# Kernel tuning notes

Hardware: AMD Instinct MI355X
Metric: run time of the kernel (lower is better)

Reference implementation:

```python
import jax, jax.numpy as jnp
import numpy as np

B, P, N, D = 8, 4, 1024, 384
H, PD = 8, 48  # num_heads, projection_dim = D // H
SCALE = float(PD ** 0.5)


def setup_inputs() -> dict:
    key = jax.random.key(0)
    ks = jax.random.split(key, 3)
    x = jax.random.normal(ks[0], (B, P, N, D), dtype=jnp.float32)
    w_qkv = jax.random.normal(ks[1], (D, H, 3 * PD), dtype=jnp.float32) * (1.0 / np.sqrt(D))
    b_qkv = jnp.zeros((H, 3 * PD), dtype=jnp.float32)
    w_o = jax.random.normal(ks[2], (PD, H, D), dtype=jnp.float32) * (1.0 / np.sqrt(PD * H))
    b_o = jnp.zeros((D,), dtype=jnp.float32)
    return {"x": x, "w_qkv": w_qkv, "b_qkv": b_qkv, "w_o": w_o, "b_o": b_o}


def reference(x, w_qkv, b_qkv, w_o, b_o):
    # QKV projection: [b,p,n,d] x [d,h,3e] -> [b,p,h,n,3e]
    qkv = jnp.einsum('bpnd,dhe->bphne', x, w_qkv) + b_qkv[None, None, :, None, :]
    q, k, v = jnp.split(qkv, 3, axis=-1)  # each [b,p,h,n,e]
    # attention over n (patches) within each (b,p,h)
    attn = jnp.einsum('bphie,bphje->bphij', q, k) / SCALE
    attn = jax.nn.softmax(attn, axis=-1)
    wv = jnp.einsum('bphij,bphje->bphie', attn, v)  # [b,p,h,n,e]
    out = jnp.einsum('bphne,ehd->bpnd', wv, w_o) + b_o
    return out
```

## Files before the change

### kernel.cpp

```cpp
#include <hip/hip_runtime.h>
#include <hip/hip_bf16.h>


#define BP 32
#define NN 1024
#define DD 384
#define HH 8
#define PDIM 48
#define E3 144
#define OO 1152
#define EP 64
#define MTOT (BP * NN)

typedef unsigned short u16;
typedef __attribute__((ext_vector_type(8))) short short8;
typedef __attribute__((ext_vector_type(4))) float f32x4;

__device__ __forceinline__ u16 f2bf(float f) {
    union { float f; unsigned int u; } v;
    v.f = f;
    unsigned int u = v.u;
    unsigned int r = u + 0x7FFFu + ((u >> 16) & 1u);
    return (u16)(r >> 16);
}

__device__ __forceinline__ void gload16(const u16* g, u16* l) {
    __builtin_amdgcn_global_load_lds(
        (const __attribute__((address_space(1))) void*)g,
        (__attribute__((address_space(3))) void*)l, 16, 0, 0);
}

__global__ void prep_kernel(const float* __restrict__ x,
                            const float* __restrict__ w_qkv,
                            const float* __restrict__ w_o,
                            u16* __restrict__ Wt, u16* __restrict__ Wot,
                            u16* __restrict__ xb) {
    int stride = gridDim.x * blockDim.x;
    int t0 = blockIdx.x * blockDim.x + threadIdx.x;
    for (int i = t0; i < OO * DD; i += stride) {
        int o = i / DD, d = i - o * DD;
        Wt[i] = f2bf(w_qkv[(size_t)d * OO + o]);
    }
    for (int i = t0; i < DD * DD; i += stride) {
        int dd = i / DD, he = i - dd * DD;
        int h = he / PDIM, e = he - h * PDIM;
        Wot[i] = f2bf(w_o[((size_t)e * HH + h) * DD + dd]);
    }
    for (int i = t0; i < MTOT * DD / 8; i += stride) {
        const float4* xp = reinterpret_cast<const float4*>(x + (size_t)i * 8);
        float4 a0 = xp[0], a1 = xp[1];
        short8 v;
        v[0] = (short)f2bf(a0.x); v[1] = (short)f2bf(a0.y);
        v[2] = (short)f2bf(a0.z); v[3] = (short)f2bf(a0.w);
        v[4] = (short)f2bf(a1.x); v[5] = (short)f2bf(a1.y);
        v[6] = (short)f2bf(a1.z); v[7] = (short)f2bf(a1.w);
        reinterpret_cast<short8*>(xb)[i] = v;
    }
}

__device__ __forceinline__ void stage_tile(const u16* __restrict__ src, int ld,
                                           u16* lds, int tid) {
#pragma unroll
    for (int i = 0; i < 4; ++i) {
        int idx = i * 256 + tid;
        int row = idx >> 3, p = idx & 7;
        int g = p ^ (row & 7);
        gload16(src + (size_t)row * ld + g * 8, lds + idx * 8);
    }
}
__device__ __forceinline__ short8 lds_frag(const u16* lds, int row, int kk, int lg) {
    int p = (kk * 4 + lg) ^ (row & 7);
    return *reinterpret_cast<const short8*>(lds + row * 64 + p * 8);
}

__global__ __launch_bounds__(256) void qkv_kernel(
    const u16* __restrict__ xb, const float* __restrict__ b_qkv,
    const u16* __restrict__ Wt,
    u16* __restrict__ q_ws, u16* __restrict__ k_ws, u16* __restrict__ vt_ws) {
    __shared__ alignas(16) u16 Al[128 * 64];
    __shared__ alignas(16) u16 Bl[128 * 64];
    int mt = blockIdx.x, nt = blockIdx.y;
    int tid = threadIdx.x;
    int w = tid >> 6, l = tid & 63, lr = l & 15, lg = l >> 4;
    int wr = w >> 1, wc = w & 1;

    const u16* Abase = xb + (size_t)mt * 128 * DD;
    const u16* Bbase = Wt + (size_t)nt * 128 * DD;

    f32x4 acc[4][4];
#pragma unroll
    for (int mi = 0; mi < 4; ++mi)
#pragma unroll
        for (int ni = 0; ni < 4; ++ni) acc[mi][ni] = (f32x4)(0.f);

#pragma unroll 1
    for (int kt = 0; kt < 6; ++kt) {
        __syncthreads();
        stage_tile(Abase + kt * 64, DD, Al, tid);
        stage_tile(Bbase + kt * 64, DD, Bl, tid);
        __syncthreads();
#pragma unroll
        for (int kk = 0; kk < 2; ++kk) {
            short8 a[4], b[4];
#pragma unroll
            for (int mi = 0; mi < 4; ++mi) a[mi] = lds_frag(Al, wr * 64 + mi * 16 + lr, kk, lg);
#pragma unroll
            for (int ni = 0; ni < 4; ++ni) b[ni] = lds_frag(Bl, wc * 64 + ni * 16 + lr, kk, lg);
#pragma unroll
            for (int mi = 0; mi < 4; ++mi)
#pragma unroll
                for (int ni = 0; ni < 4; ++ni)
                    acc[mi][ni] = __builtin_amdgcn_mfma_f32_16x16x32_bf16(a[mi], b[ni], acc[mi][ni], 0, 0, 0);
        }
    }

#pragma unroll
    for (int ni = 0; ni < 4; ++ni) {
        int o = nt * 128 + wc * 64 + ni * 16 + lr;
        int h = o / E3, e3 = o - h * E3;
        float bias = b_qkv[o];
#pragma unroll
        for (int mi = 0; mi < 4; ++mi)
#pragma unroll
            for (int r = 0; r < 4; ++r) {
                int M = mt * 128 + wr * 64 + mi * 16 + lg * 4 + r;
                int bp = M >> 10, nn = M & 1023;
                size_t bh = (size_t)bp * HH + h;
                u16 bv = f2bf(acc[mi][ni][r] + bias);
                if (e3 < 48) {
                    size_t base = (bh * NN + nn) * EP;
                    q_ws[base + e3] = bv;
                    if (e3 < 16) q_ws[base + 48 + e3] = 0;
                } else if (e3 < 96) {
                    int c = e3 - 48;
                    size_t base = (bh * NN + nn) * EP;
                    k_ws[base + c] = bv;
                    if (c < 16) k_ws[base + 48 + c] = 0;
                } else {
                    vt_ws[(bh * PDIM + (e3 - 96)) * NN + nn] = bv;
                }
            }
    }
}

__global__ __launch_bounds__(256) void attn_kernel(
    const u16* __restrict__ q_ws, const u16* __restrict__ k_ws,
    const u16* __restrict__ vt_ws, u16* __restrict__ wv_ws) {
    int rt = blockIdx.x;
    int bph = blockIdx.y;
    int bp = bph >> 3, h = bph & 7;
    int tid = threadIdx.x;
    int w = tid >> 6, l = tid & 63;
    int lr = l & 15, lg = l >> 4;

    __shared__ alignas(16) u16 Klds[64][72];
    __shared__ alignas(16) u16 Vlds[48][72];
    __shared__ alignas(16) u16 Plds[4][16][72];

    int qn = rt * 64 + w * 16 + lr;
    const u16* qrow = q_ws + ((size_t)bph * NN + qn) * EP;
    short8 aq0 = *reinterpret_cast<const short8*>(qrow + lg * 8);
    short8 aq1 = *reinterpret_cast<const short8*>(qrow + 32 + lg * 8);

    f32x4 accO[3];
#pragma unroll
    for (int i = 0; i < 3; ++i) accO[i] = (f32x4)(0.f);
    float mrun[4], lrun[4];
#pragma unroll
    for (int r = 0; r < 4; ++r) { mrun[r] = -1e30f; lrun[r] = 0.f; }
    const float inv_scale = 0.14433756729740643f;

#pragma unroll 1
    for (int jc = 0; jc < 16; ++jc) {
        {
            int j = tid >> 2, seg = (tid & 3) * 16;
            const u16* src = k_ws + ((size_t)bph * NN + jc * 64 + j) * EP + seg;
            *reinterpret_cast<short8*>(&Klds[j][seg]) = *reinterpret_cast<const short8*>(src);
            *reinterpret_cast<short8*>(&Klds[j][seg + 8]) = *reinterpret_cast<const short8*>(src + 8);
            if (tid < 192) {
                int e = tid >> 2;
                const u16* vsrc = vt_ws + ((size_t)bph * PDIM + e) * NN + jc * 64 + seg;
                *reinterpret_cast<short8*>(&Vlds[e][seg]) = *reinterpret_cast<const short8*>(vsrc);
                *reinterpret_cast<short8*>(&Vlds[e][seg + 8]) = *reinterpret_cast<const short8*>(vsrc + 8);
            }
        }
        __syncthreads();

        f32x4 s[4];
#pragma unroll
        for (int ct = 0; ct < 4; ++ct) {
            s[ct] = (f32x4)(0.f);
            short8 bk0 = *reinterpret_cast<const short8*>(&Klds[ct * 16 + lr][lg * 8]);
            short8 bk1 = *reinterpret_cast<const short8*>(&Klds[ct * 16 + lr][32 + lg * 8]);
            s[ct] = __builtin_amdgcn_mfma_f32_16x16x32_bf16(aq0, bk0, s[ct], 0, 0, 0);
            s[ct] = __builtin_amdgcn_mfma_f32_16x16x32_bf16(aq1, bk1, s[ct], 0, 0, 0);
        }
#pragma unroll
        for (int ct = 0; ct < 4; ++ct) s[ct] *= inv_scale;

        float mnew[4], alpha[4];
#pragma unroll
        for (int r = 0; r < 4; ++r) {
            float m = fmaxf(fmaxf(s[0][r], s[1][r]), fmaxf(s[2][r], s[3][r]));
#pragma unroll
            for (int off = 1; off < 16; off <<= 1) m = fmaxf(m, __shfl_xor(m, off));
            mnew[r] = fmaxf(mrun[r], m);
            alpha[r] = __expf(mrun[r] - mnew[r]);
            mrun[r] = mnew[r];
        }
        float p[4][4];
#pragma unroll
        for (int ct = 0; ct < 4; ++ct)
#pragma unroll
            for (int r = 0; r < 4; ++r) p[ct][r] = __expf(s[ct][r] - mnew[r]);
#pragma unroll
        for (int r = 0; r < 4; ++r) {
            float rs = p[0][r] + p[1][r] + p[2][r] + p[3][r];
#pragma unroll
            for (int off = 1; off < 16; off <<= 1) rs += __shfl_xor(rs, off);
            lrun[r] = lrun[r] * alpha[r] + rs;
        }
#pragma unroll
        for (int i = 0; i < 3; ++i)
#pragma unroll
            for (int r = 0; r < 4; ++r) accO[i][r] *= alpha[r];

#pragma unroll
        for (int ct = 0; ct < 4; ++ct)
#pragma unroll
            for (int r = 0; r < 4; ++r)
                Plds[w][lg * 4 + r][ct * 16 + lr] = f2bf(p[ct][r]);

#pragma unroll
        for (int kb = 0; kb < 2; ++kb) {
            short8 ap = *reinterpret_cast<const short8*>(&Plds[w][lr][kb * 32 + lg * 8]);
#pragma unroll
            for (int et = 0; et < 3; ++et) {
                short8 bv = *reinterpret_cast<const short8*>(&Vlds[et * 16 + lr][kb * 32 + lg * 8]);
                accO[et] = __builtin_amdgcn_mfma_f32_16x16x32_bf16(ap, bv, accO[et], 0, 0, 0);
            }
        }
        __syncthreads();
    }

#pragma unroll
    for (int et = 0; et < 3; ++et)
#pragma unroll
        for (int r = 0; r < 4; ++r) {
            int nn = rt * 64 + w * 16 + lg * 4 + r;
            int he = h * PDIM + et * 16 + lr;
            wv_ws[((size_t)bp * NN + nn) * DD + he] = f2bf(accO[et][r] / lrun[r]);
        }
}

__global__ __launch_bounds__(256) void oproj_kernel(
    const u16* __restrict__ wv_ws, const u16* __restrict__ Wot,
    const float* __restrict__ b_o, float* __restrict__ out) {
    __shared__ alignas(16) u16 Al[128 * 64];
    __shared__ alignas(16) u16 Bl[128 * 64];
    int mt = blockIdx.x, nt = blockIdx.y;
    int tid = threadIdx.x;
    int w = tid >> 6, l = tid & 63, lr = l & 15, lg = l >> 4;
    int wr = w >> 1, wc = w & 1;

    const u16* Abase = wv_ws + (size_t)mt * 128 * DD;
    const u16* Bbase = Wot + (size_t)nt * 128 * DD;

    f32x4 acc[4][4];
#pragma unroll
    for (int mi = 0; mi < 4; ++mi)
#pragma unroll
        for (int ni = 0; ni < 4; ++ni) acc[mi][ni] = (f32x4)(0.f);

#pragma unroll 1
    for (int kt = 0; kt < 6; ++kt) {
        __syncthreads();
        stage_tile(Abase + kt * 64, DD, Al, tid);
        stage_tile(Bbase + kt * 64, DD, Bl, tid);
        __syncthreads();
#pragma unroll
        for (int kk = 0; kk < 2; ++kk) {
            short8 a[4], b[4];
#pragma unroll
            for (int mi = 0; mi < 4; ++mi) a[mi] = lds_frag(Al, wr * 64 + mi * 16 + lr, kk, lg);
#pragma unroll
            for (int ni = 0; ni < 4; ++ni) b[ni] = lds_frag(Bl, wc * 64 + ni * 16 + lr, kk, lg);
#pragma unroll
            for (int mi = 0; mi < 4; ++mi)
#pragma unroll
                for (int ni = 0; ni < 4; ++ni)
                    acc[mi][ni] = __builtin_amdgcn_mfma_f32_16x16x32_bf16(a[mi], b[ni], acc[mi][ni], 0, 0, 0);
        }
    }

#pragma unroll
    for (int ni = 0; ni < 4; ++ni) {
        int d = nt * 128 + wc * 64 + ni * 16 + lr;
        float bo = b_o[d];
#pragma unroll
        for (int mi = 0; mi < 4; ++mi)
#pragma unroll
            for (int r = 0; r < 4; ++r) {
                int M = mt * 128 + wr * 64 + mi * 16 + lg * 4 + r;
                out[(size_t)M * DD + d] = acc[mi][ni][r] + bo;
            }
    }
}

extern "C" void kernel_launch(void* const* d_in, const int* in_sizes, int n_in,
                              void* d_out, int out_size, void* d_ws, size_t ws_size,
                              hipStream_t stream) {
    const float* x     = (const float*)d_in[0];
    const float* w_qkv = (const float*)d_in[1];
    const float* b_qkv = (const float*)d_in[2];
    const float* w_o   = (const float*)d_in[3];
    const float* b_o   = (const float*)d_in[4];
    float* out = (float*)d_out;

    char* ws = (char*)d_ws;
    size_t off = 0;
    u16* Wt    = (u16*)(ws + off); off += (size_t)OO * DD * 2;
    u16* Wot   = (u16*)(ws + off); off += (size_t)DD * DD * 2;
    u16* q_ws  = (u16*)(ws + off); off += (size_t)BP * HH * NN * EP * 2;
    u16* k_ws  = (u16*)(ws + off); off += (size_t)BP * HH * NN * EP * 2;
    u16* vt_ws = (u16*)(ws + off); off += (size_t)BP * HH * PDIM * NN * 2;
    u16* wv_ws = (u16*)(ws + off); off += (size_t)BP * NN * DD * 2;
    u16* xb    = wv_ws;
    (void)ws_size;

    prep_kernel<<<2048, 256, 0, stream>>>(x, w_qkv, w_o, Wt, Wot, xb);
    qkv_kernel<<<dim3(256, 9), 256, 0, stream>>>(xb, b_qkv, Wt, q_ws, k_ws, vt_ws);
    attn_kernel<<<dim3(16, 256), 256, 0, stream>>>(q_ws, k_ws, vt_ws, wv_ws);
    oproj_kernel<<<dim3(256, 3), 256, 0, stream>>>(wv_ws, Wot, b_o, out);
}
```

Baseline: 408.1 us.

## Restructure attention: 128-row tiles, async swizzled LDS loads, lazy softmax rescale

Each attention workgroup now handles 128 query rows instead of 64, with each wave holding two 16-row Q fragments. Every K/V fragment read from LDS therefore feeds two MFMAs, and the number of K/V tile loads per query is halved. K and V tiles are staged with direct global-to-LDS loads into an XOR-swizzled layout, which removes the padding; V rows are padded to 64 so the loads come out uniform. The softmax scale is folded into Q inside the QKV epilogue, and the running-max rescale is skipped when the new max exceeds the old one by no more than 8. The grid is also remapped to a 1D block order spread across XCDs, at the cost of a larger V workspace and more registers per thread.

```diff
diff --git a/kernel.cpp b/kernel.cpp
--- a/kernel.cpp
+++ b/kernel.cpp
@@ -10,6 +10,7 @@
 #define E3 144
 #define OO 1152
 #define EP 64
+#define VROWS 64
 #define MTOT (BP * NN)
 
 typedef unsigned short u16;
@@ -22,6 +23,12 @@
     unsigned int u = v.u;
     unsigned int r = u + 0x7FFFu + ((u >> 16) & 1u);
     return (u16)(r >> 16);
+}
+
+__device__ __forceinline__ u16 f2bf_hw(float f) {
+    union { __hip_bfloat16 b; u16 u; } v;
+    v.b = __float2bfloat16(f);
+    return v.u;
 }
 
 __device__ __forceinline__ void gload16(const u16* g, u16* l) {
@@ -114,6 +121,7 @@
         }
     }
 
+    const float inv_scale = 0.14433756729740643f;
 #pragma unroll
     for (int ni = 0; ni < 4; ++ni) {
         int o = nt * 128 + wc * 64 + ni * 16 + lr;
@@ -126,18 +134,18 @@
                 int M = mt * 128 + wr * 64 + mi * 16 + lg * 4 + r;
                 int bp = M >> 10, nn = M & 1023;
                 size_t bh = (size_t)bp * HH + h;
-                u16 bv = f2bf(acc[mi][ni][r] + bias);
+                float val = acc[mi][ni][r] + bias;
                 if (e3 < 48) {
                     size_t base = (bh * NN + nn) * EP;
-                    q_ws[base + e3] = bv;
+                    q_ws[base + e3] = f2bf(val * inv_scale);
                     if (e3 < 16) q_ws[base + 48 + e3] = 0;
                 } else if (e3 < 96) {
                     int c = e3 - 48;
                     size_t base = (bh * NN + nn) * EP;
-                    k_ws[base + c] = bv;
+                    k_ws[base + c] = f2bf(val);
                     if (c < 16) k_ws[base + 48 + c] = 0;
                 } else {
-                    vt_ws[(bh * PDIM + (e3 - 96)) * NN + nn] = bv;
+                    vt_ws[(bh * VROWS + (e3 - 96)) * NN + nn] = f2bf(val);
                 }
             }
     }
@@ -146,111 +154,133 @@
 __global__ __launch_bounds__(256) void attn_kernel(
     const u16* __restrict__ q_ws, const u16* __restrict__ k_ws,
     const u16* __restrict__ vt_ws, u16* __restrict__ wv_ws) {
-    int rt = blockIdx.x;
-    int bph = blockIdx.y;
-    int bp = bph >> 3, h = bph & 7;
+    int bid = blockIdx.x;
+    int wgid = (bid & 7) * 256 + (bid >> 3);
+    int bph = wgid >> 3, rt = wgid & 7;
+    int bp = bph >> 3, hd = bph & 7;
     int tid = threadIdx.x;
-    int w = tid >> 6, l = tid & 63;
-    int lr = l & 15, lg = l >> 4;
-
-    __shared__ alignas(16) u16 Klds[64][72];
-    __shared__ alignas(16) u16 Vlds[48][72];
-    __shared__ alignas(16) u16 Plds[4][16][72];
-
-    int qn = rt * 64 + w * 16 + lr;
-    const u16* qrow = q_ws + ((size_t)bph * NN + qn) * EP;
-    short8 aq0 = *reinterpret_cast<const short8*>(qrow + lg * 8);
-    short8 aq1 = *reinterpret_cast<const short8*>(qrow + 32 + lg * 8);
-
-    f32x4 accO[3];
-#pragma unroll
-    for (int i = 0; i < 3; ++i) accO[i] = (f32x4)(0.f);
-    float mrun[4], lrun[4];
-#pragma unroll
-    for (int r = 0; r < 4; ++r) { mrun[r] = -1e30f; lrun[r] = 0.f; }
-    const float inv_scale = 0.14433756729740643f;
+    int w = tid >> 6, l = tid & 63, lr = l & 15, lg = l >> 4;
+
+    __shared__ alignas(16) u16 Klds[64 * 64];
+    __shared__ alignas(16) u16 Vlds[64 * 64];
+    __shared__ alignas(16) u16 Plds[4][32][72];
+
+    short8 aq[2][2];
+#pragma unroll
+    for (int hh = 0; hh < 2; ++hh) {
+        const u16* qrow = q_ws + ((size_t)bph * NN + rt * 128 + w * 32 + hh * 16 + lr) * EP;
+        aq[hh][0] = *reinterpret_cast<const short8*>(qrow + lg * 8);
+        aq[hh][1] = *reinterpret_cast<const short8*>(qrow + 32 + lg * 8);
+    }
+
+    f32x4 accO[2][3];
+#pragma unroll
+    for (int hh = 0; hh < 2; ++hh)
+#pragma unroll
+        for (int et = 0; et < 3; ++et) accO[hh][et] = (f32x4)(0.f);
+    float mrun[2][4], lrun[2][4];
+#pragma unroll
+    for (int hh = 0; hh < 2; ++hh)
+#pragma unroll
+        for (int r = 0; r < 4; ++r) { mrun[hh][r] = -1e30f; lrun[hh][r] = 0.f; }
 
 #pragma unroll 1
     for (int jc = 0; jc < 16; ++jc) {
-        {
-            int j = tid >> 2, seg = (tid & 3) * 16;
-            const u16* src = k_ws + ((size_t)bph * NN + jc * 64 + j) * EP + seg;
-            *reinterpret_cast<short8*>(&Klds[j][seg]) = *reinterpret_cast<const short8*>(src);
-            *reinterpret_cast<short8*>(&Klds[j][seg + 8]) = *reinterpret_cast<const short8*>(src + 8);
-            if (tid < 192) {
-                int e = tid >> 2;
-                const u16* vsrc = vt_ws + ((size_t)bph * PDIM + e) * NN + jc * 64 + seg;
-                *reinterpret_cast<short8*>(&Vlds[e][seg]) = *reinterpret_cast<const short8*>(vsrc);
-                *reinterpret_cast<short8*>(&Vlds[e][seg + 8]) = *reinterpret_cast<const short8*>(vsrc + 8);
-            }
-        }
-        __syncthreads();
-
-        f32x4 s[4];
-#pragma unroll
-        for (int ct = 0; ct < 4; ++ct) {
-            s[ct] = (f32x4)(0.f);
-            short8 bk0 = *reinterpret_cast<const short8*>(&Klds[ct * 16 + lr][lg * 8]);
-            short8 bk1 = *reinterpret_cast<const short8*>(&Klds[ct * 16 + lr][32 + lg * 8]);
-            s[ct] = __builtin_amdgcn_mfma_f32_16x16x32_bf16(aq0, bk0, s[ct], 0, 0, 0);
-            s[ct] = __builtin_amdgcn_mfma_f32_16x16x32_bf16(aq1, bk1, s[ct], 0, 0, 0);
-        }
-#pragma unroll
-        for (int ct = 0; ct < 4; ++ct) s[ct] *= inv_scale;
-
-        float mnew[4], alpha[4];
-#pragma unroll
-        for (int r = 0; r < 4; ++r) {
-            float m = fmaxf(fmaxf(s[0][r], s[1][r]), fmaxf(s[2][r], s[3][r]));
-#pragma unroll
-            for (int off = 1; off < 16; off <<= 1) m = fmaxf(m, __shfl_xor(m, off));
-            mnew[r] = fmaxf(mrun[r], m);
-            alpha[r] = __expf(mrun[r] - mnew[r]);
-            mrun[r] = mnew[r];
-        }
-        float p[4][4];
+#pragma unroll
+        for (int i = 0; i < 2; ++i) {
+            int idx = i * 256 + tid, row = idx >> 3, p = idx & 7;
+            int g = p ^ (row & 7);
+            gload16(k_ws + ((size_t)bph * NN + jc * 64 + row) * EP + g * 8, Klds + idx * 8);
+            gload16(vt_ws + ((size_t)bph * VROWS + row) * NN + jc * 64 + g * 8, Vlds + idx * 8);
+        }
+        __syncthreads();
+
+        f32x4 s[2][4];
+#pragma unroll
+        for (int hh = 0; hh < 2; ++hh)
+#pragma unroll
+            for (int ct = 0; ct < 4; ++ct) s[hh][ct] = (f32x4)(0.f);
 #pragma unroll
         for (int ct = 0; ct < 4; ++ct)
 #pragma unroll
-            for (int r = 0; r < 4; ++r) p[ct][r] = __expf(s[ct][r] - mnew[r]);
-#pragma unroll
-        for (int r = 0; r < 4; ++r) {
-            float rs = p[0][r] + p[1][r] + p[2][r] + p[3][r];
-#pragma unroll
-            for (int off = 1; off < 16; off <<= 1) rs += __shfl_xor(rs, off);
-            lrun[r] = lrun[r] * alpha[r] + rs;
-        }
-#pragma unroll
-        for (int i = 0; i < 3; ++i)
-#pragma unroll
-            for (int r = 0; r < 4; ++r) accO[i][r] *= alpha[r];
-
-#pragma unroll
-        for (int ct = 0; ct < 4; ++ct)
-#pragma unroll
-            for (int r = 0; r < 4; ++r)
-                Plds[w][lg * 4 + r][ct * 16 + lr] = f2bf(p[ct][r]);
+            for (int kk = 0; kk < 2; ++kk) {
+                short8 bk = lds_frag(Klds, ct * 16 + lr, kk, lg);
+#pragma unroll
+                for (int hh = 0; hh < 2; ++hh)
+                    s[hh][ct] = __builtin_amdgcn_mfma_f32_16x16x32_bf16(aq[hh][kk], bk, s[hh][ct], 0, 0, 0);
+            }
+
+        float pmax[2][4];
+        bool stable = true;
+#pragma unroll
+        for (int hh = 0; hh < 2; ++hh)
+#pragma unroll
+            for (int r = 0; r < 4; ++r) {
+                float m = fmaxf(fmaxf(s[hh][0][r], s[hh][1][r]), fmaxf(s[hh][2][r], s[hh][3][r]));
+#pragma unroll
+                for (int off = 1; off < 16; off <<= 1) m = fmaxf(m, __shfl_xor(m, off));
+                pmax[hh][r] = m;
+                stable = stable && (m <= mrun[hh][r] + 8.f);
+            }
+        if (!__all(stable)) {
+#pragma unroll
+            for (int hh = 0; hh < 2; ++hh)
+#pragma unroll
+                for (int r = 0; r < 4; ++r) {
+                    float mnew = fmaxf(mrun[hh][r], pmax[hh][r]);
+                    float alpha = __expf(mrun[hh][r] - mnew);
+                    mrun[hh][r] = mnew;
+                    lrun[hh][r] *= alpha;
+#pragma unroll
+                    for (int et = 0; et < 3; ++et) accO[hh][et][r] *= alpha;
+                }
+        }
+#pragma unroll
+        for (int hh = 0; hh < 2; ++hh)
+#pragma unroll
+            for (int r = 0; r < 4; ++r) {
+#pragma unroll
+                for (int ct = 0; ct < 4; ++ct) s[hh][ct][r] = __expf(s[hh][ct][r] - mrun[hh][r]);
+                float rs = s[hh][0][r] + s[hh][1][r] + s[hh][2][r] + s[hh][3][r];
+#pragma unroll
+                for (int off = 1; off < 16; off <<= 1) rs += __shfl_xor(rs, off);
+                lrun[hh][r] += rs;
+            }
+#pragma unroll
+        for (int hh = 0; hh < 2; ++hh)
+#pragma unroll
+            for (int ct = 0; ct < 4; ++ct)
+#pragma unroll
+                for (int r = 0; r < 4; ++r)
+                    Plds[w][hh * 16 + lg * 4 + r][ct * 16 + lr] = f2bf_hw(s[hh][ct][r]);
 
 #pragma unroll
         for (int kb = 0; kb < 2; ++kb) {
-            short8 ap = *reinterpret_cast<const short8*>(&Plds[w][lr][kb * 32 + lg * 8]);
+            short8 ap[2];
+#pragma unroll
+            for (int hh = 0; hh < 2; ++hh)
+                ap[hh] = *reinterpret_cast<const short8*>(&Plds[w][hh * 16 + lr][kb * 32 + lg * 8]);
 #pragma unroll
             for (int et = 0; et < 3; ++et) {
-                short8 bv = *reinterpret_cast<const short8*>(&Vlds[et * 16 + lr][kb * 32 + lg * 8]);
-                accO[et] = __builtin_amdgcn_mfma_f32_16x16x32_bf16(ap, bv, accO[et], 0, 0, 0);
-            }
-        }
-        __syncthreads();
-    }
-
-#pragma unroll
-    for (int et = 0; et < 3; ++et)
-#pragma unroll
-        for (int r = 0; r < 4; ++r) {
-            int nn = rt * 64 + w * 16 + lg * 4 + r;
-            int he = h * PDIM + et * 16 + lr;
-            wv_ws[((size_t)bp * NN + nn) * DD + he] = f2bf(accO[et][r] / lrun[r]);
-        }
+                short8 bv = lds_frag(Vlds, et * 16 + lr, kb, lg);
+#pragma unroll
+                for (int hh = 0; hh < 2; ++hh)
+                    accO[hh][et] = __builtin_amdgcn_mfma_f32_16x16x32_bf16(ap[hh], bv, accO[hh][et], 0, 0, 0);
+            }
+        }
+        __syncthreads();
+    }
+
+#pragma unroll
+    for (int hh = 0; hh < 2; ++hh)
+#pragma unroll
+        for (int et = 0; et < 3; ++et)
+#pragma unroll
+            for (int r = 0; r < 4; ++r) {
+                int nn = rt * 128 + w * 32 + hh * 16 + lg * 4 + r;
+                int he = hd * PDIM + et * 16 + lr;
+                wv_ws[((size_t)bp * NN + nn) * DD + he] = f2bf(accO[hh][et][r] / lrun[hh][r]);
+            }
 }
 
 __global__ __launch_bounds__(256) void oproj_kernel(
@@ -323,13 +353,13 @@
     u16* Wot   = (u16*)(ws + off); off += (size_t)DD * DD * 2;
     u16* q_ws  = (u16*)(ws + off); off += (size_t)BP * HH * NN * EP * 2;
     u16* k_ws  = (u16*)(ws + off); off += (size_t)BP * HH * NN * EP * 2;
-    u16* vt_ws = (u16*)(ws + off); off += (size_t)BP * HH * PDIM * NN * 2;
+    u16* vt_ws = (u16*)(ws + off); off += (size_t)BP * HH * VROWS * NN * 2;
     u16* wv_ws = (u16*)(ws + off); off += (size_t)BP * NN * DD * 2;
     u16* xb    = wv_ws;
     (void)ws_size;
 
     prep_kernel<<<2048, 256, 0, stream>>>(x, w_qkv, w_o, Wt, Wot, xb);
     qkv_kernel<<<dim3(256, 9), 256, 0, stream>>>(xb, b_qkv, Wt, q_ws, k_ws, vt_ws);
-    attn_kernel<<<dim3(16, 256), 256, 0, stream>>>(q_ws, k_ws, vt_ws, wv_ws);
+    attn_kernel<<<2048, 256, 0, stream>>>(q_ws, k_ws, vt_ws, wv_ws);
     oproj_kernel<<<dim3(256, 3), 256, 0, stream>>>(wv_ws, Wot, b_o, out);
 }
```

Result: slower. 422.3 us (+3.5%).
